# Optimization experiments

Measured on AMD Instinct MI355X. Metric: run time of the kernel, lower is better.

## Reference

```python
import jax, jax.numpy as jnp
import numpy as np

N_U, N_I, D = 30000, 15000, 64
L = 2                 # propagation layers (self.l)
TEMP = 0.2
LAMBDA1, LAMBDA2 = 0.2, 1e-7
H, F = 4, 16          # GAT heads x per-head dim; H*F == D
NEG_SLOPE = 0.2
AVG_DEG = 16
B = 2048


def setup_inputs() -> dict:
    key = jax.random.key(0)
    ks = jax.random.split(key, 10)
    rng = np.random.default_rng(0)
    E_u_0 = jax.random.normal(ks[0], (N_U, D), jnp.float32) * 0.1
    E_i_0 = jax.random.normal(ks[1], (N_I, D), jnp.float32) * 0.1
    # sparse normalized bipartite adjacency (adj_norm) as an edge list
    nnz = N_U * AVG_DEG
    u_idx = np.repeat(np.arange(N_U), AVG_DEG)
    i_idx = rng.integers(0, N_I, nnz)
    deg_u = np.bincount(u_idx, minlength=N_U)
    deg_i = np.maximum(np.bincount(i_idx, minlength=N_I), 1)
    vals = (1.0 / np.sqrt(deg_u[u_idx] * deg_i[i_idx])).astype(np.float32)
    # GAT graph on n_u+n_i nodes: bipartite edges both directions + self-loops
    n = N_U + N_I
    src = np.concatenate([u_idx, i_idx + N_U, np.arange(n)]).astype(np.int32)
    dst = np.concatenate([i_idx + N_U, u_idx, np.arange(n)]).astype(np.int32)
    # GAT parameters (fresh each forward in original, so just random)
    W = jax.random.normal(ks[2], (D, H * F), jnp.float32) / np.sqrt(D)
    attn_l = jax.random.normal(ks[3], (H, F), jnp.float32) * 0.1
    attn_r = jax.random.normal(ks[4], (H, F), jnp.float32) * 0.1
    uids = jax.random.randint(ks[5], (B,), 0, N_U, jnp.int32)
    iids = jax.random.randint(ks[6], (B,), 0, N_I, jnp.int32)
    pos = jax.random.randint(ks[7], (B,), 0, N_I, jnp.int32)
    neg = jax.random.randint(ks[8], (B,), 0, N_I, jnp.int32)
    return dict(E_u_0=E_u_0, E_i_0=E_i_0, adj_vals=jnp.asarray(vals),
                W=W, attn_l=attn_l, attn_r=attn_r,
                u_idx=jnp.asarray(u_idx, jnp.int32), i_idx=jnp.asarray(i_idx, jnp.int32),
                src=jnp.asarray(src), dst=jnp.asarray(dst),
                uids=uids, iids=iids, pos=pos, neg=neg)


def gat_layer(h, src, dst, W, attn_l, attn_r, n_nodes):
    # GATConv: project, per-edge attention, neighborhood softmax, scatter-agg
    feat = (h @ W).reshape(-1, H, F)                      # [N,H,F]
    el = (feat * attn_l).sum(-1)                          # [N,H]
    er = (feat * attn_r).sum(-1)                          # [N,H]
    e = jax.nn.leaky_relu(el[src] + er[dst], NEG_SLOPE)   # [E,H]
    e_max = jax.ops.segment_max(e, dst, num_segments=n_nodes)
    a = jnp.exp(e - e_max[dst])
    denom = jax.ops.segment_sum(a, dst, num_segments=n_nodes)
    a = a / denom[dst]                                    # self-loops => denom>0
    out = jax.ops.segment_sum(a[:, :, None] * feat[src], dst, num_segments=n_nodes)
    return jax.nn.elu(out.reshape(-1, H * F))             # [N,D]


def _forward(E_u_0, E_i_0, adj_vals, W, attn_l, attn_r,
             u_idx, i_idx, src, dst, uids, iids, pos, neg):
    n = N_U + N_I
    Eu, Ei = E_u_0, E_i_0
    sum_Eu, sum_Ei = E_u_0, E_i_0
    sum_Gu, sum_Gi = E_u_0, E_i_0
    for _ in range(L):
        # LightGCN spmm propagation: Z_u = A @ E_i, Z_i = A.T @ E_u
        Zu = jax.ops.segment_sum(adj_vals[:, None] * Ei[i_idx], u_idx, num_segments=N_U)
        Zi = jax.ops.segment_sum(adj_vals[:, None] * Eu[u_idx], i_idx, num_segments=N_I)
        ls1 = gat_layer(jnp.concatenate([Eu, Ei], 0), src, dst, W, attn_l, attn_r, n)
        Gu, Gi = ls1[:N_U], ls1[N_U:]
        Eu, Ei = Zu + Eu, Zi + Ei
        sum_Eu = sum_Eu + Eu
        sum_Ei = sum_Ei + Ei
        sum_Gu = sum_Gu + Gu
        sum_Gi = sum_Gi + Gi
    log_eps = jnp.float32(np.log(1e-8))
    # InfoNCE: log(sum(exp(s)) + 1e-8) == logaddexp(logsumexp(s), log(1e-8))
    lse_u = jax.scipy.special.logsumexp(sum_Gu[uids] @ sum_Eu.T / TEMP, axis=1)
    lse_i = jax.scipy.special.logsumexp(sum_Gi[iids] @ sum_Ei.T / TEMP, axis=1)
    neg_score = jnp.logaddexp(lse_u, log_eps).mean() + jnp.logaddexp(lse_i, log_eps).mean()
    pos_score = ((sum_Gu[uids] * sum_Eu[uids]).sum(1) / TEMP).mean() \
              + ((sum_Gi[iids] * sum_Ei[iids]).sum(1) / TEMP).mean()
    loss_s = -pos_score + neg_score
    # BPR loss
    u_emb = sum_Eu[uids]
    diff = (u_emb * sum_Ei[pos]).sum(-1) - (u_emb * sum_Ei[neg]).sum(-1)
    loss_r = -jax.nn.log_sigmoid(diff).mean()
    # L2 reg over nn.Parameters (E_u_0, E_i_0 only)
    loss_reg = LAMBDA2 * ((E_u_0 ** 2).sum() + (E_i_0 ** 2).sum())
    loss = loss_r + LAMBDA1 * loss_s + loss_reg
    return loss, loss_r, LAMBDA1 * loss_s


def reference(E_u_0, E_i_0, adj_vals, W, attn_l, attn_r,
              u_idx, i_idx, src, dst, uids, iids, pos, neg):
    return _forward(E_u_0, E_i_0, adj_vals, W, attn_l, attn_r,
                    u_idx, i_idx, src, dst, uids, iids, pos, neg)
```

## Files before the change

kernel.cpp:

```cpp
#include <hip/hip_runtime.h>
#include <math.h>

#define N_U 30000
#define N_I 15000
#define N_TOT 45000
#define D 64
#define NNZ 480000
#define B 2048
#define INV_TEMP 5.0f
#define LOG_EPS -18.420680743952367f
#define NEG_SLOPE 0.2f
#define LAMBDA1 0.2f
#define LAMBDA2 1e-7f

#define NSP 128
#define RSP_U 235
#define RSP_I 118
#define PAD_U 30016
#define PAD_I 15040
#define SCALE_LOG2 7.2134752044448170f
#define LN2F 0.6931471805599453f

typedef __attribute__((ext_vector_type(8))) short short8;
typedef __attribute__((ext_vector_type(4))) float f32x4;

__device__ inline float wred(float v) {
#pragma unroll
  for (int o = 32; o > 0; o >>= 1) v += __shfl_down(v, o, 64);
  return v;
}

__device__ inline float leaky(float v) { return (v >= 0.f) ? v : NEG_SLOPE * v; }

__device__ inline void atomMaxF(float* a, float v) {
  if (v >= 0.f) atomicMax((int*)a, __float_as_int(v));
  else atomicMin((unsigned int*)a, __float_as_uint(v));
}

__device__ inline unsigned short f2bf(float x) {
  unsigned u = __float_as_uint(x);
  unsigned r = u + 0x7FFFu + ((u >> 16) & 1u);
  return (unsigned short)(r >> 16);
}
__device__ inline float bf2f(unsigned short h) {
  return __uint_as_float(((unsigned)h) << 16);
}

__global__ void k_init(const float* __restrict__ Eu0, const float* __restrict__ Ei0,
                       float* fU, float* fI, float* sEu, float* sEi,
                       float* sGu, float* sGi, int* deg, float* acc) {
  int t = blockIdx.x * 256 + threadIdx.x;
  if (t < 16) acc[t] = (t >= 8) ? -INFINITY : 0.f;
  if (t < N_I) deg[t] = 0;
  if (t < N_U * D) {
    int n = t >> 6, c = t & 63;
    float v = Eu0[t];
    fU[(size_t)n * 128 + c] = v;
    sEu[t] = v; sGu[t] = v;
  } else if (t < N_TOT * D) {
    int j = t - N_U * D;
    int n = j >> 6, c = j & 63;
    float v = Ei0[j];
    fI[(size_t)n * 128 + c] = v;
    sEi[j] = v; sGi[j] = v;
  }
}

__global__ void k_deg(const int* __restrict__ ii, int* deg) {
  int e = blockIdx.x * 256 + threadIdx.x;
  if (e < NNZ) atomicAdd(&deg[ii[e]], 1);
}

__global__ void k_scan(const int* __restrict__ deg, int* rowptr, int* cursor) {
  __shared__ int buf[1024];
  __shared__ int carry;
  int tid = threadIdx.x;
  if (tid == 0) carry = 0;
  __syncthreads();
  for (int base = 0; base < N_I; base += 1024) {
    int v = (base + tid < N_I) ? deg[base + tid] : 0;
    buf[tid] = v;
    __syncthreads();
    for (int o = 1; o < 1024; o <<= 1) {
      int x = (tid >= o) ? buf[tid - o] : 0;
      __syncthreads();
      buf[tid] += x;
      __syncthreads();
    }
    if (base + tid < N_I) {
      int excl = carry + buf[tid] - v;
      rowptr[base + tid] = excl;
      cursor[base + tid] = excl;
    }
    __syncthreads();
    if (tid == 1023) carry += buf[1023];
    __syncthreads();
  }
  if (tid == 0) rowptr[N_I] = carry;
}

__global__ void k_fill(const int* __restrict__ ii, const float* __restrict__ vals,
                       int* cursor, int* u_srt, float* v_srt) {
  int e = blockIdx.x * 256 + threadIdx.x;
  if (e < NNZ) {
    int pos = atomicAdd(&cursor[ii[e]], 1);
    u_srt[pos] = e >> 4;
    v_srt[pos] = vals[e];
  }
}

__global__ void k_feat(float* __restrict__ fU, float* __restrict__ fI,
                       const float* __restrict__ W, const float* __restrict__ al,
                       const float* __restrict__ ar,
                       float* __restrict__ el, float* __restrict__ er) {
  __shared__ float Ws[64 * 64];
  __shared__ float hs[16][64];
  int tid = threadIdx.x;
  for (int t = tid; t < 1024; t += 256) ((float4*)Ws)[t] = ((const float4*)W)[t];
  int g = tid >> 6, c = tid & 63;
  int n0 = blockIdx.x * 16 + g * 4;
  float* rows[4];
#pragma unroll
  for (int j = 0; j < 4; j++) {
    int node = n0 + j;
    rows[j] = nullptr;
    if (node < N_TOT) {
      rows[j] = (node < N_U) ? (fU + (size_t)node * 128) : (fI + (size_t)(node - N_U) * 128);
      hs[g * 4 + j][c] = rows[j][c];
    }
  }
  __syncthreads();
  float a0 = 0.f, a1 = 0.f, a2 = 0.f, a3 = 0.f;
#pragma unroll 8
  for (int k = 0; k < 64; ++k) {
    float w = Ws[k * 64 + c];
    a0 = fmaf(hs[g * 4 + 0][k], w, a0);
    a1 = fmaf(hs[g * 4 + 1][k], w, a1);
    a2 = fmaf(hs[g * 4 + 2][k], w, a2);
    a3 = fmaf(hs[g * 4 + 3][k], w, a3);
  }
  float accs[4] = {a0, a1, a2, a3};
  float alc = al[c], arc = ar[c];
#pragma unroll
  for (int j = 0; j < 4; j++) {
    int node = n0 + j;
    if (node >= N_TOT) continue;
    rows[j][64 + c] = accs[j];
    float pl = accs[j] * alc;
    float pr = accs[j] * arc;
#pragma unroll
    for (int o = 8; o >= 1; o >>= 1) {
      pl += __shfl_down(pl, o, 16);
      pr += __shfl_down(pr, o, 16);
    }
    if ((c & 15) == 0) {
      el[node * 4 + (c >> 4)] = pl;
      er[node * 4 + (c >> 4)] = pr;
    }
  }
}

__global__ void k_elmax(const float* __restrict__ el, float* __restrict__ dst) {
  __shared__ float red[4][4];
  int tid = threadIdx.x;
  int lane = tid & 63, wv = tid >> 6;
  float mx = -INFINITY;
  for (int t = blockIdx.x * 256 + tid; t < N_TOT * 4; t += 64 * 256)
    mx = fmaxf(mx, el[t]);
#pragma unroll
  for (int o = 4; o < 64; o <<= 1) mx = fmaxf(mx, __shfl_xor(mx, o, 64));
  if (lane < 4) red[wv][lane] = mx;
  __syncthreads();
  if (tid < 4) {
    float m2 = fmaxf(fmaxf(red[0][tid], red[1][tid]), fmaxf(red[2][tid], red[3][tid]));
    atomMaxF(dst + tid, m2);
  }
}

__global__ void k_user_layer(const float* __restrict__ fU_cur, const float* __restrict__ fI_cur,
                             const float* __restrict__ el, const float* __restrict__ er,
                             const float* __restrict__ vals, const int* __restrict__ ii,
                             const float* __restrict__ elmx,
                             float* __restrict__ fU_nxt, float* __restrict__ sEu,
                             float* __restrict__ sGu,
                             unsigned short* __restrict__ EH, unsigned short* __restrict__ EL,
                             float* __restrict__ normArr) {
  int t = blockIdx.x * 256 + threadIdx.x;
  int u = t >> 6, c = t & 63;
  if (u >= N_U) return;
  int h = c >> 4;
  float eru = er[u * 4 + h];
  float m = leaky(elmx[h] + eru);
  const float* selfrow = fU_cur + (size_t)u * 128;
  float aself = __expf(leaky(el[u * 4 + h] + eru) - m);

  int idx[16]; float vv[16];
#pragma unroll
  for (int k = 0; k < 16; k++) { idx[k] = ii[u * 16 + k]; vv[k] = vals[u * 16 + k]; }
  float av[16];
#pragma unroll
  for (int k = 0; k < 16; k++)
    av[k] = __expf(leaky(el[(idx[k] + N_U) * 4 + h] + eru) - m);

  float den = aself;
#pragma unroll
  for (int k = 0; k < 16; k++) den += av[k];

  float o0 = aself * selfrow[64 + c], o1 = 0.f;
  float z0 = 0.f, z1 = 0.f;
#pragma unroll
  for (int k = 0; k < 16; k += 2) {
    const float* rA = fI_cur + (size_t)idx[k] * 128;
    const float* rB = fI_cur + (size_t)idx[k + 1] * 128;
    float eA = rA[c], fA = rA[64 + c];
    float eB = rB[c], fB = rB[64 + c];
    z0 = fmaf(vv[k], eA, z0);
    z1 = fmaf(vv[k + 1], eB, z1);
    o0 = fmaf(av[k], fA, o0);
    o1 = fmaf(av[k + 1], fB, o1);
  }
  float o = (o0 + o1) / den;
  float g = (o > 0.f) ? o : expm1f(o);
  float e_new = selfrow[c] + z0 + z1;
  fU_nxt[(size_t)u * 128 + c] = e_new;
  size_t off = (size_t)u * D + c;
  float s_final = sEu[off] + e_new;
  sEu[off] = s_final;
  sGu[off] += g;
  if (EH) {
    unsigned short hi = f2bf(s_final);
    EH[off] = hi;
    EL[off] = f2bf(s_final - bf2f(hi));
    float n2 = wred(s_final * s_final);
    if (c == 0) normArr[u] = n2;
  }
}

__global__ void k_item_layer(const float* __restrict__ fU_cur, const float* __restrict__ fI_cur,
                             const float* __restrict__ el, const float* __restrict__ er,
                             const int* __restrict__ rowptr, const int* __restrict__ u_srt,
                             const float* __restrict__ v_srt,
                             const float* __restrict__ elmx,
                             float* __restrict__ fI_nxt, float* __restrict__ sEi,
                             float* __restrict__ sGi,
                             unsigned short* __restrict__ EH, unsigned short* __restrict__ EL,
                             float* __restrict__ normArr) {
  int t = blockIdx.x * 256 + threadIdx.x;
  int i = t >> 6, c = t & 63;
  if (i >= N_I) return;
  int h = c >> 4;
  int node = N_U + i;
  float eri = er[node * 4 + h];
  float m = leaky(elmx[h] + eri);
  const float* selfrow = fI_cur + (size_t)i * 128;
  float aself = __expf(leaky(el[node * 4 + h] + eri) - m);
  float den0 = aself, den1 = 0.f;
  float o0 = aself * selfrow[64 + c], o1 = 0.f;
  float z0 = 0.f, z1 = 0.f;
  int r0 = rowptr[i], r1 = rowptr[i + 1];
  int r = r0;
  for (; r + 3 < r1; r += 4) {
    int u0 = u_srt[r], u1 = u_srt[r + 1], u2 = u_srt[r + 2], u3 = u_srt[r + 3];
    float v0 = v_srt[r], v1 = v_srt[r + 1], v2 = v_srt[r + 2], v3 = v_srt[r + 3];
    float a0 = __expf(leaky(el[u0 * 4 + h] + eri) - m);
    float a1 = __expf(leaky(el[u1 * 4 + h] + eri) - m);
    float a2 = __expf(leaky(el[u2 * 4 + h] + eri) - m);
    float a3 = __expf(leaky(el[u3 * 4 + h] + eri) - m);
    const float* R0 = fU_cur + (size_t)u0 * 128;
    const float* R1 = fU_cur + (size_t)u1 * 128;
    const float* R2 = fU_cur + (size_t)u2 * 128;
    const float* R3 = fU_cur + (size_t)u3 * 128;
    float e0 = R0[c], f0 = R0[64 + c];
    float e1 = R1[c], f1 = R1[64 + c];
    float e2 = R2[c], f2 = R2[64 + c];
    float e3 = R3[c], f3 = R3[64 + c];
    z0 = fmaf(v0, e0, z0); z1 = fmaf(v1, e1, z1);
    z0 = fmaf(v2, e2, z0); z1 = fmaf(v3, e3, z1);
    den0 += a0 + a2; den1 += a1 + a3;
    o0 = fmaf(a0, f0, o0); o1 = fmaf(a1, f1, o1);
    o0 = fmaf(a2, f2, o0); o1 = fmaf(a3, f3, o1);
  }
  for (; r < r1; r++) {
    int u0 = u_srt[r];
    float v0 = v_srt[r];
    float a0 = __expf(leaky(el[u0 * 4 + h] + eri) - m);
    const float* R0 = fU_cur + (size_t)u0 * 128;
    float e0 = R0[c], f0 = R0[64 + c];
    z0 = fmaf(v0, e0, z0);
    den0 += a0;
    o0 = fmaf(a0, f0, o0);
  }
  float o = (o0 + o1) / (den0 + den1);
  float g = (o > 0.f) ? o : expm1f(o);
  float e_new = selfrow[c] + z0 + z1;
  fI_nxt[(size_t)i * 128 + c] = e_new;
  size_t off = (size_t)i * D + c;
  float s_final = sEi[off] + e_new;
  sEi[off] = s_final;
  sGi[off] += g;
  if (EH) {
    unsigned short hi = f2bf(s_final);
    EH[off] = hi;
    EL[off] = f2bf(s_final - bf2f(hi));
    float n2 = wred(s_final * s_final);
    if (c == 0) normArr[i] = n2;
  }
}

__global__ void k_norm_max(const float* __restrict__ nU, const float* __restrict__ nI,
                           float* __restrict__ acc) {
  __shared__ float red[4][2];
  int tid = threadIdx.x;
  int lane = tid & 63, wv = tid >> 6;
  float mu = 0.f, mi = 0.f;
  for (int t = blockIdx.x * 256 + tid; t < N_U; t += 64 * 256) mu = fmaxf(mu, nU[t]);
  for (int t = blockIdx.x * 256 + tid; t < N_I; t += 64 * 256) mi = fmaxf(mi, nI[t]);
#pragma unroll
  for (int o = 32; o > 0; o >>= 1) {
    mu = fmaxf(mu, __shfl_down(mu, o, 64));
    mi = fmaxf(mi, __shfl_down(mi, o, 64));
  }
  if (lane == 0) { red[wv][0] = mu; red[wv][1] = mi; }
  __syncthreads();
  if (tid == 0) {
    float a = fmaxf(fmaxf(red[0][0], red[1][0]), fmaxf(red[2][0], red[3][0]));
    float b = fmaxf(fmaxf(red[0][1], red[1][1]), fmaxf(red[2][1], red[3][1]));
    atomMaxF(acc + 6, a);
    atomMaxF(acc + 7, b);
  }
}

__global__ void k_cvt_q(const float* __restrict__ sGu, const float* __restrict__ sGi,
                        const int* __restrict__ uids, const int* __restrict__ iids,
                        unsigned short* __restrict__ QuH, unsigned short* __restrict__ QuL,
                        unsigned short* __restrict__ QiH, unsigned short* __restrict__ QiL,
                        const float* __restrict__ acc,
                        float* __restrict__ M0u, float* __restrict__ M0i) {
  int lane = threadIdx.x & 63, wv = threadIdx.x >> 6;
  int row = blockIdx.x * 4 + wv;
  int side = row >> 11;
  int b = row & (B - 1);
  int id = side ? iids[b] : uids[b];
  float x = (side ? sGi : sGu)[(size_t)id * 64 + lane] * SCALE_LOG2;
  unsigned short hi = f2bf(x);
  unsigned short lo = f2bf(x - bf2f(hi));
  if (side) { QiH[(size_t)b * 64 + lane] = hi; QiL[(size_t)b * 64 + lane] = lo; }
  else      { QuH[(size_t)b * 64 + lane] = hi; QuL[(size_t)b * 64 + lane] = lo; }
  float n2 = wred(x * x);
  if (lane == 0) {
    float en2 = side ? acc[7] : acc[6];
    float M0 = sqrtf(n2) * sqrtf(en2) * 1.01f + 1.0f;
    (side ? M0i : M0u)[b] = M0;
  }
}

__global__ __launch_bounds__(256, 2) void k_lse_mfma(
    const unsigned short* __restrict__ Qhi, const unsigned short* __restrict__ Qlo,
    const unsigned short* __restrict__ Ehi, const unsigned short* __restrict__ Elo,
    const float* __restrict__ M0arr,
    int n_rows, int rows_per_split,
    float* __restrict__ part_s) {
  int tid = threadIdx.x;
  int wave = tid >> 6, lane = tid & 63;
  int l15 = lane & 15, quad = lane >> 4;
  int qbase = (blockIdx.x * 4 + wave) * 128;
  int split = blockIdx.y;
  int row0 = split * rows_per_split;
  int row_end = min(row0 + rows_per_split, n_rows);
  int rows = row_end - row0; if (rows < 0) rows = 0;
  int total = (rows + 15) >> 4;
  int ntail = rows & 15;

  float ss[8][4];
#pragma unroll
  for (int t = 0; t < 8; t++)
#pragma unroll
    for (int g = 0; g < 4; g++) ss[t][g] = 0.f;

  if (total > 0) {
    short8 ah[8][2], al[8][2];
#pragma unroll
    for (int t = 0; t < 8; t++)
#pragma unroll
      for (int c = 0; c < 2; c++) {
        size_t idx = (size_t)(qbase + t * 16 + l15) * 64 + c * 32 + quad * 8;
        ah[t][c] = *(const short8*)(Qhi + idx);
        al[t][c] = *(const short8*)(Qlo + idx);
      }

    f32x4 cinit[8];
#pragma unroll
    for (int t = 0; t < 8; t++)
#pragma unroll
      for (int g = 0; g < 4; g++)
        cinit[t][g] = -M0arr[qbase + t * 16 + quad * 4 + g];

    const unsigned short* ph = Ehi + (size_t)(row0 + l15) * 64 + quad * 8;
    const unsigned short* pl = Elo + (size_t)(row0 + l15) * 64 + quad * 8;

    short8 cb0 = *(const short8*)(ph);
    short8 cb1 = *(const short8*)(ph + 32);
    short8 cb2 = *(const short8*)(pl);
    short8 cb3 = *(const short8*)(pl + 32);
    ph += 1024; pl += 1024;

    for (int it = 0; it < total - 1; it++) {
      short8 nb0 = *(const short8*)(ph);
      short8 nb1 = *(const short8*)(ph + 32);
      short8 nb2 = *(const short8*)(pl);
      short8 nb3 = *(const short8*)(pl + 32);
      ph += 1024; pl += 1024;
#pragma unroll
      for (int t = 0; t < 8; t++) {
        f32x4 acc = cinit[t];
        acc = __builtin_amdgcn_mfma_f32_16x16x32_bf16(ah[t][0], cb0, acc, 0, 0, 0);
        acc = __builtin_amdgcn_mfma_f32_16x16x32_bf16(ah[t][1], cb1, acc, 0, 0, 0);
        acc = __builtin_amdgcn_mfma_f32_16x16x32_bf16(al[t][0], cb0, acc, 0, 0, 0);
        acc = __builtin_amdgcn_mfma_f32_16x16x32_bf16(al[t][1], cb1, acc, 0, 0, 0);
        acc = __builtin_amdgcn_mfma_f32_16x16x32_bf16(ah[t][0], cb2, acc, 0, 0, 0);
        acc = __builtin_amdgcn_mfma_f32_16x16x32_bf16(ah[t][1], cb3, acc, 0, 0, 0);
#pragma unroll
        for (int g = 0; g < 4; g++)
          ss[t][g] += exp2f(acc[g]);
      }
      cb0 = nb0; cb1 = nb1; cb2 = nb2; cb3 = nb3;
    }
    {
      bool valid = (ntail == 0) || (l15 < ntail);
#pragma unroll
      for (int t = 0; t < 8; t++) {
        f32x4 acc = cinit[t];
        acc = __builtin_amdgcn_mfma_f32_16x16x32_bf16(ah[t][0], cb0, acc, 0, 0, 0);
        acc = __builtin_amdgcn_mfma_f32_16x16x32_bf16(ah[t][1], cb1, acc, 0, 0, 0);
        acc = __builtin_amdgcn_mfma_f32_16x16x32_bf16(al[t][0], cb0, acc, 0, 0, 0);
        acc = __builtin_amdgcn_mfma_f32_16x16x32_bf16(al[t][1], cb1, acc, 0, 0, 0);
        acc = __builtin_amdgcn_mfma_f32_16x16x32_bf16(ah[t][0], cb2, acc, 0, 0, 0);
        acc = __builtin_amdgcn_mfma_f32_16x16x32_bf16(ah[t][1], cb3, acc, 0, 0, 0);
#pragma unroll
        for (int g = 0; g < 4; g++) {
          float e = exp2f(acc[g]);
          ss[t][g] += valid ? e : 0.f;
        }
      }
    }
  }

#pragma unroll
  for (int off = 1; off < 16; off <<= 1) {
#pragma unroll
    for (int t = 0; t < 8; t++)
#pragma unroll
      for (int g = 0; g < 4; g++)
        ss[t][g] += __shfl_xor(ss[t][g], off, 64);
  }

  if (l15 == 0) {
#pragma unroll
    for (int t = 0; t < 8; t++)
#pragma unroll
      for (int g = 0; g < 4; g++) {
        int q = qbase + t * 16 + quad * 4 + g;
        part_s[(size_t)split * B + q] = ss[t][g];
      }
  }
}

__global__ void k_reg(const float* __restrict__ Eu0, const float* __restrict__ Ei0, float* acc) {
  __shared__ float red[4];
  int tid = threadIdx.x;
  float s = 0.f;
  const float4* A = (const float4*)Eu0;
  const float4* Bp = (const float4*)Ei0;
  const int nA = N_U * 16, nTot = N_TOT * 16;
  for (int t = blockIdx.x * 256 + tid; t < nTot; t += 256 * 256) {
    float4 v = (t < nA) ? A[t] : Bp[t - nA];
    s += v.x * v.x + v.y * v.y + v.z * v.z + v.w * v.w;
  }
  s = wred(s);
  if ((tid & 63) == 0) red[tid >> 6] = s;
  __syncthreads();
  if (tid == 0) unsafeAtomicAdd(acc + 5, red[0] + red[1] + red[2] + red[3]);
}

__global__ void k_small(const float* __restrict__ sEu, const float* __restrict__ sEi,
                        const float* __restrict__ sGu, const float* __restrict__ sGi,
                        const int* __restrict__ uids, const int* __restrict__ iids,
                        const int* __restrict__ pos, const int* __restrict__ neg,
                        const float* __restrict__ psU, const float* __restrict__ psI,
                        const float* __restrict__ M0u, const float* __restrict__ M0i,
                        float* acc) {
  int b = blockIdx.x * 256 + threadIdx.x;
  float du = 0.f, di = 0.f, nu = 0.f, ni = 0.f, bpr = 0.f;
  if (b < B) {
    float su = 0.f, si = 0.f;
    for (int s2 = 0; s2 < NSP; s2++) su += psU[(size_t)s2 * B + b];
    for (int s2 = 0; s2 < NSP; s2++) si += psI[(size_t)s2 * B + b];
    float lseu = M0u[b] * LN2F + logf(su);
    float lsei = M0i[b] * LN2F + logf(si);
    nu = fmaxf(lseu, LOG_EPS) + log1pf(expf(-fabsf(lseu - LOG_EPS)));
    ni = fmaxf(lsei, LOG_EPS) + log1pf(expf(-fabsf(lsei - LOG_EPS)));

    int u = uids[b], it = iids[b], p = pos[b], ng = neg[b];
    const float4* gu = (const float4*)(sGu + (size_t)u * D);
    const float4* eu = (const float4*)(sEu + (size_t)u * D);
    const float4* gi = (const float4*)(sGi + (size_t)it * D);
    const float4* ei = (const float4*)(sEi + (size_t)it * D);
    const float4* ep = (const float4*)(sEi + (size_t)p * D);
    const float4* en = (const float4*)(sEi + (size_t)ng * D);
    float diff = 0.f;
#pragma unroll
    for (int k = 0; k < 16; k++) {
      float4 a = gu[k], b4 = eu[k];
      du += a.x * b4.x + a.y * b4.y + a.z * b4.z + a.w * b4.w;
      float4 c = gi[k], d4 = ei[k];
      di += c.x * d4.x + c.y * d4.y + c.z * d4.z + c.w * d4.w;
      float4 e = ep[k], f = en[k];
      diff += b4.x * (e.x - f.x) + b4.y * (e.y - f.y) + b4.z * (e.z - f.z) + b4.w * (e.w - f.w);
    }
    bpr = (diff > 0.f) ? log1pf(expf(-diff)) : (-diff + log1pf(expf(diff)));
  }
  du = wred(du); di = wred(di); nu = wred(nu); ni = wred(ni); bpr = wred(bpr);
  if ((threadIdx.x & 63) == 0) {
    unsafeAtomicAdd(acc + 0, du);
    unsafeAtomicAdd(acc + 1, di);
    unsafeAtomicAdd(acc + 2, nu);
    unsafeAtomicAdd(acc + 3, ni);
    unsafeAtomicAdd(acc + 4, bpr);
  }
}

__global__ void k_final(const float* __restrict__ acc, float* __restrict__ out) {
  float pos_score = (acc[0] + acc[1]) * (INV_TEMP / (float)B);
  float neg_score = (acc[2] + acc[3]) / (float)B;
  float loss_s = neg_score - pos_score;
  float loss_r = acc[4] / (float)B;
  float reg = LAMBDA2 * acc[5];
  out[0] = loss_r + LAMBDA1 * loss_s + reg;
  out[1] = loss_r;
  out[2] = LAMBDA1 * loss_s;
}

extern "C" void kernel_launch(void* const* d_in, const int* in_sizes, int n_in,
                              void* d_out, int out_size, void* d_ws, size_t ws_size,
                              hipStream_t stream) {
  const float* Eu0  = (const float*)d_in[0];
  const float* Ei0  = (const float*)d_in[1];
  const float* vals = (const float*)d_in[2];
  const float* W    = (const float*)d_in[3];
  const float* al   = (const float*)d_in[4];
  const float* ar   = (const float*)d_in[5];
  const int* ii     = (const int*)d_in[7];
  const int* uids   = (const int*)d_in[10];
  const int* iids   = (const int*)d_in[11];
  const int* pos    = (const int*)d_in[12];
  const int* neg    = (const int*)d_in[13];
  float* out = (float*)d_out;

  char* base = (char*)d_ws;
  size_t off = 0;
  auto alloc = [&](size_t bytes) -> void* {
    void* p = base + off;
    off = (off + bytes + 255) & ~(size_t)255;
    return p;
  };
  float* fU_a = (float*)alloc((size_t)N_U * 128 * 4);
  float* fU_b = (float*)alloc((size_t)N_U * 128 * 4);
  float* fI_a = (float*)alloc((size_t)N_I * 128 * 4);
  float* fI_b = (float*)alloc((size_t)N_I * 128 * 4);
  float* sEu  = (float*)alloc((size_t)N_U * D * 4);
  float* sEi  = (float*)alloc((size_t)N_I * D * 4);
  float* sGu  = (float*)alloc((size_t)N_U * D * 4);
  float* sGi  = (float*)alloc((size_t)N_I * D * 4);
  float* el   = (float*)alloc((size_t)N_TOT * 4 * 4);
  float* er   = (float*)alloc((size_t)N_TOT * 4 * 4);
  float* psU  = (float*)alloc((size_t)B * NSP * 4);
  float* psI  = (float*)alloc((size_t)B * NSP * 4);
  float* M0u  = (float*)alloc((size_t)B * 4);
  float* M0i  = (float*)alloc((size_t)B * 4);
  float* normU= (float*)alloc((size_t)N_U * 4);
  float* normI= (float*)alloc((size_t)N_I * 4);
  float* acc  = (float*)alloc(16 * 4);
  int* deg    = (int*)alloc((size_t)N_I * 4);
  int* cursor = (int*)alloc((size_t)N_I * 4);
  int* rowptr = (int*)alloc((size_t)(N_I + 1) * 4);
  int* u_srt  = (int*)alloc((size_t)NNZ * 4);
  float* v_srt= (float*)alloc((size_t)NNZ * 4);
  unsigned short* EuH = (unsigned short*)alloc((size_t)PAD_U * 64 * 2);
  unsigned short* EuL = (unsigned short*)alloc((size_t)PAD_U * 64 * 2);
  unsigned short* EiH = (unsigned short*)alloc((size_t)PAD_I * 64 * 2);
  unsigned short* EiL = (unsigned short*)alloc((size_t)PAD_I * 64 * 2);
  unsigned short* QuH = (unsigned short*)alloc((size_t)B * 64 * 2);
  unsigned short* QuL = (unsigned short*)alloc((size_t)B * 64 * 2);
  unsigned short* QiH = (unsigned short*)alloc((size_t)B * 64 * 2);
  unsigned short* QiL = (unsigned short*)alloc((size_t)B * 64 * 2);

  k_init<<<(N_TOT * D + 255) / 256, 256, 0, stream>>>(Eu0, Ei0, fU_a, fI_a, sEu, sEi, sGu, sGi,
                                                      deg, acc);
  k_deg<<<(NNZ + 255) / 256, 256, 0, stream>>>(ii, deg);
  k_scan<<<1, 1024, 0, stream>>>(deg, rowptr, cursor);
  k_fill<<<(NNZ + 255) / 256, 256, 0, stream>>>(ii, vals, cursor, u_srt, v_srt);

  float* cu = fU_a; float* ci = fI_a;
  float* nu = fU_b; float* ni = fI_b;
  for (int l = 0; l < 2; ++l) {
    float* elmx = acc + 8 + 4 * l;
    bool last = (l == 1);
    k_feat<<<(N_TOT + 15) / 16, 256, 0, stream>>>(cu, ci, W, al, ar, el, er);
    k_elmax<<<64, 256, 0, stream>>>(el, elmx);
    k_user_layer<<<(N_U * D) / 256, 256, 0, stream>>>(cu, ci, el, er, vals, ii, elmx, nu, sEu, sGu,
                                                      last ? EuH : nullptr, last ? EuL : nullptr,
                                                      normU);
    k_item_layer<<<(N_I * D) / 256, 256, 0, stream>>>(cu, ci, el, er, rowptr, u_srt, v_srt, elmx,
                                                      ni, sEi, sGi,
                                                      last ? EiH : nullptr, last ? EiL : nullptr,
                                                      normI);
    float* t1 = cu; cu = nu; nu = t1;
    float* t2 = ci; ci = ni; ni = t2;
  }

  k_norm_max<<<64, 256, 0, stream>>>(normU, normI, acc);
  k_cvt_q<<<(2 * B) / 4, 256, 0, stream>>>(sGu, sGi, uids, iids, QuH, QuL, QiH, QiL, acc, M0u, M0i);
  k_lse_mfma<<<dim3(B / 512, NSP), 256, 0, stream>>>(QuH, QuL, EuH, EuL, M0u, N_U, RSP_U, psU);
  k_lse_mfma<<<dim3(B / 512, NSP), 256, 0, stream>>>(QiH, QiL, EiH, EiL, M0i, N_I, RSP_I, psI);
  k_reg<<<256, 256, 0, stream>>>(Eu0, Ei0, acc);
  k_small<<<B / 256, 256, 0, stream>>>(sEu, sEi, sGu, sGi, uids, iids, pos, neg,
                                       psU, psI, M0u, M0i, acc);
  k_final<<<1, 1, 0, stream>>>(acc, out);
}
```

Measured before the change: 464.3 us.

## Merge per-layer user/item kernels, fuse reg into norm-max, batch LSE launches

Combines the user and item propagation kernels into one launch covering all nodes. Folds the L2 regularization sum into the norm-max reduction kernel, and launches both LSE MFMA passes as a single grid using blockIdx.z. Also rewrites the degree scan so each thread sums a chunk of 15 elements, replacing the serial 15-pass block scan. The aim is to cut launch count and tail idle time between small kernels. The cost is branch divergence at the user/item boundary and more registers held in the merged kernel.

```diff
diff --git a/kernel.cpp b/kernel.cpp
--- a/kernel.cpp
+++ b/kernel.cpp
@@ -72,31 +72,35 @@
 }
 
 __global__ void k_scan(const int* __restrict__ deg, int* rowptr, int* cursor) {
-  __shared__ int buf[1024];
-  __shared__ int carry;
+  __shared__ int tsum[1024];
+  const int CHUNK = 15;
   int tid = threadIdx.x;
-  if (tid == 0) carry = 0;
+  int base = tid * CHUNK;
+  int s = 0;
+#pragma unroll
+  for (int k = 0; k < CHUNK; k++) {
+    int idx = base + k;
+    s += (idx < N_I) ? deg[idx] : 0;
+  }
+  tsum[tid] = s;
   __syncthreads();
-  for (int base = 0; base < N_I; base += 1024) {
-    int v = (base + tid < N_I) ? deg[base + tid] : 0;
-    buf[tid] = v;
+  for (int o = 1; o < 1024; o <<= 1) {
+    int x = (tid >= o) ? tsum[tid - o] : 0;
     __syncthreads();
-    for (int o = 1; o < 1024; o <<= 1) {
-      int x = (tid >= o) ? buf[tid - o] : 0;
-      __syncthreads();
-      buf[tid] += x;
-      __syncthreads();
-    }
-    if (base + tid < N_I) {
-      int excl = carry + buf[tid] - v;
-      rowptr[base + tid] = excl;
-      cursor[base + tid] = excl;
-    }
+    tsum[tid] += x;
     __syncthreads();
-    if (tid == 1023) carry += buf[1023];
-    __syncthreads();
-  }
-  if (tid == 0) rowptr[N_I] = carry;
+  }
+  int excl = tsum[tid] - s;
+#pragma unroll
+  for (int k = 0; k < CHUNK; k++) {
+    int idx = base + k;
+    if (idx < N_I) {
+      rowptr[idx] = excl;
+      cursor[idx] = excl;
+      excl += deg[idx];
+    }
+  }
+  if (tid == 1023) rowptr[N_I] = tsum[1023];
 }
 
 __global__ void k_fill(const int* __restrict__ ii, const float* __restrict__ vals,
@@ -177,156 +181,161 @@
   }
 }
 
-__global__ void k_user_layer(const float* __restrict__ fU_cur, const float* __restrict__ fI_cur,
-                             const float* __restrict__ el, const float* __restrict__ er,
-                             const float* __restrict__ vals, const int* __restrict__ ii,
-                             const float* __restrict__ elmx,
-                             float* __restrict__ fU_nxt, float* __restrict__ sEu,
-                             float* __restrict__ sGu,
-                             unsigned short* __restrict__ EH, unsigned short* __restrict__ EL,
-                             float* __restrict__ normArr) {
+__global__ void k_layer(const float* __restrict__ fU_cur, const float* __restrict__ fI_cur,
+                        const float* __restrict__ el, const float* __restrict__ er,
+                        const float* __restrict__ vals, const int* __restrict__ ii,
+                        const int* __restrict__ rowptr, const int* __restrict__ u_srt,
+                        const float* __restrict__ v_srt,
+                        const float* __restrict__ elmx,
+                        float* __restrict__ fU_nxt, float* __restrict__ fI_nxt,
+                        float* __restrict__ sEu, float* __restrict__ sEi,
+                        float* __restrict__ sGu, float* __restrict__ sGi,
+                        unsigned short* __restrict__ EuH, unsigned short* __restrict__ EuL,
+                        unsigned short* __restrict__ EiH, unsigned short* __restrict__ EiL,
+                        float* __restrict__ normU, float* __restrict__ normI) {
   int t = blockIdx.x * 256 + threadIdx.x;
-  int u = t >> 6, c = t & 63;
-  if (u >= N_U) return;
+  int node = t >> 6, c = t & 63;
+  if (node >= N_TOT) return;
   int h = c >> 4;
-  float eru = er[u * 4 + h];
-  float m = leaky(elmx[h] + eru);
-  const float* selfrow = fU_cur + (size_t)u * 128;
-  float aself = __expf(leaky(el[u * 4 + h] + eru) - m);
-
-  int idx[16]; float vv[16];
-#pragma unroll
-  for (int k = 0; k < 16; k++) { idx[k] = ii[u * 16 + k]; vv[k] = vals[u * 16 + k]; }
-  float av[16];
-#pragma unroll
-  for (int k = 0; k < 16; k++)
-    av[k] = __expf(leaky(el[(idx[k] + N_U) * 4 + h] + eru) - m);
-
-  float den = aself;
-#pragma unroll
-  for (int k = 0; k < 16; k++) den += av[k];
-
-  float o0 = aself * selfrow[64 + c], o1 = 0.f;
-  float z0 = 0.f, z1 = 0.f;
-#pragma unroll
-  for (int k = 0; k < 16; k += 2) {
-    const float* rA = fI_cur + (size_t)idx[k] * 128;
-    const float* rB = fI_cur + (size_t)idx[k + 1] * 128;
-    float eA = rA[c], fA = rA[64 + c];
-    float eB = rB[c], fB = rB[64 + c];
-    z0 = fmaf(vv[k], eA, z0);
-    z1 = fmaf(vv[k + 1], eB, z1);
-    o0 = fmaf(av[k], fA, o0);
-    o1 = fmaf(av[k + 1], fB, o1);
-  }
-  float o = (o0 + o1) / den;
-  float g = (o > 0.f) ? o : expm1f(o);
-  float e_new = selfrow[c] + z0 + z1;
-  fU_nxt[(size_t)u * 128 + c] = e_new;
-  size_t off = (size_t)u * D + c;
-  float s_final = sEu[off] + e_new;
-  sEu[off] = s_final;
-  sGu[off] += g;
-  if (EH) {
-    unsigned short hi = f2bf(s_final);
-    EH[off] = hi;
-    EL[off] = f2bf(s_final - bf2f(hi));
-    float n2 = wred(s_final * s_final);
-    if (c == 0) normArr[u] = n2;
-  }
-}
-
-__global__ void k_item_layer(const float* __restrict__ fU_cur, const float* __restrict__ fI_cur,
-                             const float* __restrict__ el, const float* __restrict__ er,
-                             const int* __restrict__ rowptr, const int* __restrict__ u_srt,
-                             const float* __restrict__ v_srt,
-                             const float* __restrict__ elmx,
-                             float* __restrict__ fI_nxt, float* __restrict__ sEi,
-                             float* __restrict__ sGi,
-                             unsigned short* __restrict__ EH, unsigned short* __restrict__ EL,
-                             float* __restrict__ normArr) {
-  int t = blockIdx.x * 256 + threadIdx.x;
-  int i = t >> 6, c = t & 63;
-  if (i >= N_I) return;
-  int h = c >> 4;
-  int node = N_U + i;
-  float eri = er[node * 4 + h];
-  float m = leaky(elmx[h] + eri);
-  const float* selfrow = fI_cur + (size_t)i * 128;
-  float aself = __expf(leaky(el[node * 4 + h] + eri) - m);
-  float den0 = aself, den1 = 0.f;
-  float o0 = aself * selfrow[64 + c], o1 = 0.f;
-  float z0 = 0.f, z1 = 0.f;
-  int r0 = rowptr[i], r1 = rowptr[i + 1];
-  int r = r0;
-  for (; r + 3 < r1; r += 4) {
-    int u0 = u_srt[r], u1 = u_srt[r + 1], u2 = u_srt[r + 2], u3 = u_srt[r + 3];
-    float v0 = v_srt[r], v1 = v_srt[r + 1], v2 = v_srt[r + 2], v3 = v_srt[r + 3];
-    float a0 = __expf(leaky(el[u0 * 4 + h] + eri) - m);
-    float a1 = __expf(leaky(el[u1 * 4 + h] + eri) - m);
-    float a2 = __expf(leaky(el[u2 * 4 + h] + eri) - m);
-    float a3 = __expf(leaky(el[u3 * 4 + h] + eri) - m);
-    const float* R0 = fU_cur + (size_t)u0 * 128;
-    const float* R1 = fU_cur + (size_t)u1 * 128;
-    const float* R2 = fU_cur + (size_t)u2 * 128;
-    const float* R3 = fU_cur + (size_t)u3 * 128;
-    float e0 = R0[c], f0 = R0[64 + c];
-    float e1 = R1[c], f1 = R1[64 + c];
-    float e2 = R2[c], f2 = R2[64 + c];
-    float e3 = R3[c], f3 = R3[64 + c];
-    z0 = fmaf(v0, e0, z0); z1 = fmaf(v1, e1, z1);
-    z0 = fmaf(v2, e2, z0); z1 = fmaf(v3, e3, z1);
-    den0 += a0 + a2; den1 += a1 + a3;
-    o0 = fmaf(a0, f0, o0); o1 = fmaf(a1, f1, o1);
-    o0 = fmaf(a2, f2, o0); o1 = fmaf(a3, f3, o1);
-  }
-  for (; r < r1; r++) {
-    int u0 = u_srt[r];
-    float v0 = v_srt[r];
-    float a0 = __expf(leaky(el[u0 * 4 + h] + eri) - m);
-    const float* R0 = fU_cur + (size_t)u0 * 128;
-    float e0 = R0[c], f0 = R0[64 + c];
-    z0 = fmaf(v0, e0, z0);
-    den0 += a0;
-    o0 = fmaf(a0, f0, o0);
-  }
-  float o = (o0 + o1) / (den0 + den1);
-  float g = (o > 0.f) ? o : expm1f(o);
-  float e_new = selfrow[c] + z0 + z1;
-  fI_nxt[(size_t)i * 128 + c] = e_new;
-  size_t off = (size_t)i * D + c;
-  float s_final = sEi[off] + e_new;
-  sEi[off] = s_final;
-  sGi[off] += g;
-  if (EH) {
-    unsigned short hi = f2bf(s_final);
-    EH[off] = hi;
-    EL[off] = f2bf(s_final - bf2f(hi));
-    float n2 = wred(s_final * s_final);
-    if (c == 0) normArr[i] = n2;
-  }
-}
-
-__global__ void k_norm_max(const float* __restrict__ nU, const float* __restrict__ nI,
-                           float* __restrict__ acc) {
-  __shared__ float red[4][2];
+
+  if (node < N_U) {
+    int u = node;
+    float eru = er[u * 4 + h];
+    float m = leaky(elmx[h] + eru);
+    const float* selfrow = fU_cur + (size_t)u * 128;
+    float aself = __expf(leaky(el[u * 4 + h] + eru) - m);
+
+    int idx[16]; float vv[16];
+#pragma unroll
+    for (int k = 0; k < 16; k++) { idx[k] = ii[u * 16 + k]; vv[k] = vals[u * 16 + k]; }
+    float av[16];
+#pragma unroll
+    for (int k = 0; k < 16; k++)
+      av[k] = __expf(leaky(el[(idx[k] + N_U) * 4 + h] + eru) - m);
+
+    float den = aself;
+#pragma unroll
+    for (int k = 0; k < 16; k++) den += av[k];
+
+    float o0 = aself * selfrow[64 + c], o1 = 0.f;
+    float z0 = 0.f, z1 = 0.f;
+#pragma unroll
+    for (int k = 0; k < 16; k += 2) {
+      const float* rA = fI_cur + (size_t)idx[k] * 128;
+      const float* rB = fI_cur + (size_t)idx[k + 1] * 128;
+      float eA = rA[c], fA = rA[64 + c];
+      float eB = rB[c], fB = rB[64 + c];
+      z0 = fmaf(vv[k], eA, z0);
+      z1 = fmaf(vv[k + 1], eB, z1);
+      o0 = fmaf(av[k], fA, o0);
+      o1 = fmaf(av[k + 1], fB, o1);
+    }
+    float o = (o0 + o1) / den;
+    float g = (o > 0.f) ? o : expm1f(o);
+    float e_new = selfrow[c] + z0 + z1;
+    fU_nxt[(size_t)u * 128 + c] = e_new;
+    size_t off = (size_t)u * D + c;
+    float s_final = sEu[off] + e_new;
+    sEu[off] = s_final;
+    sGu[off] += g;
+    if (EuH) {
+      unsigned short hi = f2bf(s_final);
+      EuH[off] = hi;
+      EuL[off] = f2bf(s_final - bf2f(hi));
+      float n2 = wred(s_final * s_final);
+      if (c == 0) normU[u] = n2;
+    }
+  } else {
+    int i = node - N_U;
+    float eri = er[node * 4 + h];
+    float m = leaky(elmx[h] + eri);
+    const float* selfrow = fI_cur + (size_t)i * 128;
+    float aself = __expf(leaky(el[node * 4 + h] + eri) - m);
+    float den0 = aself, den1 = 0.f;
+    float o0 = aself * selfrow[64 + c], o1 = 0.f;
+    float z0 = 0.f, z1 = 0.f;
+    int r0 = rowptr[i], r1 = rowptr[i + 1];
+    int r = r0;
+    for (; r + 3 < r1; r += 4) {
+      int u0 = u_srt[r], u1 = u_srt[r + 1], u2 = u_srt[r + 2], u3 = u_srt[r + 3];
+      float v0 = v_srt[r], v1 = v_srt[r + 1], v2 = v_srt[r + 2], v3 = v_srt[r + 3];
+      float a0 = __expf(leaky(el[u0 * 4 + h] + eri) - m);
+      float a1 = __expf(leaky(el[u1 * 4 + h] + eri) - m);
+      float a2 = __expf(leaky(el[u2 * 4 + h] + eri) - m);
+      float a3 = __expf(leaky(el[u3 * 4 + h] + eri) - m);
+      const float* R0 = fU_cur + (size_t)u0 * 128;
+      const float* R1 = fU_cur + (size_t)u1 * 128;
+      const float* R2 = fU_cur + (size_t)u2 * 128;
+      const float* R3 = fU_cur + (size_t)u3 * 128;
+      float e0 = R0[c], f0 = R0[64 + c];
+      float e1 = R1[c], f1 = R1[64 + c];
+      float e2 = R2[c], f2 = R2[64 + c];
+      float e3 = R3[c], f3 = R3[64 + c];
+      z0 = fmaf(v0, e0, z0); z1 = fmaf(v1, e1, z1);
+      z0 = fmaf(v2, e2, z0); z1 = fmaf(v3, e3, z1);
+      den0 += a0 + a2; den1 += a1 + a3;
+      o0 = fmaf(a0, f0, o0); o1 = fmaf(a1, f1, o1);
+      o0 = fmaf(a2, f2, o0); o1 = fmaf(a3, f3, o1);
+    }
+    for (; r < r1; r++) {
+      int u0 = u_srt[r];
+      float v0 = v_srt[r];
+      float a0 = __expf(leaky(el[u0 * 4 + h] + eri) - m);
+      const float* R0 = fU_cur + (size_t)u0 * 128;
+      float e0 = R0[c], f0 = R0[64 + c];
+      z0 = fmaf(v0, e0, z0);
+      den0 += a0;
+      o0 = fmaf(a0, f0, o0);
+    }
+    float o = (o0 + o1) / (den0 + den1);
+    float g = (o > 0.f) ? o : expm1f(o);
+    float e_new = selfrow[c] + z0 + z1;
+    fI_nxt[(size_t)i * 128 + c] = e_new;
+    size_t off = (size_t)i * D + c;
+    float s_final = sEi[off] + e_new;
+    sEi[off] = s_final;
+    sGi[off] += g;
+    if (EiH) {
+      unsigned short hi = f2bf(s_final);
+      EiH[off] = hi;
+      EiL[off] = f2bf(s_final - bf2f(hi));
+      float n2 = wred(s_final * s_final);
+      if (c == 0) normI[i] = n2;
+    }
+  }
+}
+
+__global__ void k_normreg(const float* __restrict__ nU, const float* __restrict__ nI,
+                          const float* __restrict__ Eu0, const float* __restrict__ Ei0,
+                          float* __restrict__ acc) {
+  __shared__ float red[4][3];
   int tid = threadIdx.x;
   int lane = tid & 63, wv = tid >> 6;
-  float mu = 0.f, mi = 0.f;
-  for (int t = blockIdx.x * 256 + tid; t < N_U; t += 64 * 256) mu = fmaxf(mu, nU[t]);
-  for (int t = blockIdx.x * 256 + tid; t < N_I; t += 64 * 256) mi = fmaxf(mi, nI[t]);
+  float mu = 0.f, mi = 0.f, s = 0.f;
+  for (int t = blockIdx.x * 256 + tid; t < N_U; t += 128 * 256) mu = fmaxf(mu, nU[t]);
+  for (int t = blockIdx.x * 256 + tid; t < N_I; t += 128 * 256) mi = fmaxf(mi, nI[t]);
+  const float4* A = (const float4*)Eu0;
+  const float4* Bp = (const float4*)Ei0;
+  const int nA = N_U * 16, nTot = N_TOT * 16;
+  for (int t = blockIdx.x * 256 + tid; t < nTot; t += 128 * 256) {
+    float4 v = (t < nA) ? A[t] : Bp[t - nA];
+    s += v.x * v.x + v.y * v.y + v.z * v.z + v.w * v.w;
+  }
 #pragma unroll
   for (int o = 32; o > 0; o >>= 1) {
     mu = fmaxf(mu, __shfl_down(mu, o, 64));
     mi = fmaxf(mi, __shfl_down(mi, o, 64));
-  }
-  if (lane == 0) { red[wv][0] = mu; red[wv][1] = mi; }
+    s += __shfl_down(s, o, 64);
+  }
+  if (lane == 0) { red[wv][0] = mu; red[wv][1] = mi; red[wv][2] = s; }
   __syncthreads();
   if (tid == 0) {
     float a = fmaxf(fmaxf(red[0][0], red[1][0]), fmaxf(red[2][0], red[3][0]));
     float b = fmaxf(fmaxf(red[0][1], red[1][1]), fmaxf(red[2][1], red[3][1]));
+    float ssum = red[0][2] + red[1][2] + red[2][2] + red[3][2];
     atomMaxF(acc + 6, a);
     atomMaxF(acc + 7, b);
+    unsafeAtomicAdd(acc + 5, ssum);
   }
 }
 
@@ -355,11 +364,22 @@
 }
 
 __global__ __launch_bounds__(256, 2) void k_lse_mfma(
-    const unsigned short* __restrict__ Qhi, const unsigned short* __restrict__ Qlo,
-    const unsigned short* __restrict__ Ehi, const unsigned short* __restrict__ Elo,
-    const float* __restrict__ M0arr,
-    int n_rows, int rows_per_split,
-    float* __restrict__ part_s) {
+    const unsigned short* __restrict__ QuH, const unsigned short* __restrict__ QuL,
+    const unsigned short* __restrict__ EuHp, const unsigned short* __restrict__ EuLp,
+    const unsigned short* __restrict__ QiH, const unsigned short* __restrict__ QiL,
+    const unsigned short* __restrict__ EiHp, const unsigned short* __restrict__ EiLp,
+    const float* __restrict__ M0u, const float* __restrict__ M0i,
+    float* __restrict__ psU, float* __restrict__ psI) {
+  int z = blockIdx.z;
+  const unsigned short* Qhi = z ? QiH : QuH;
+  const unsigned short* Qlo = z ? QiL : QuL;
+  const unsigned short* Ehi = z ? EiHp : EuHp;
+  const unsigned short* Elo = z ? EiLp : EuLp;
+  const float* M0arr = z ? M0i : M0u;
+  float* part_s = z ? psI : psU;
+  int n_rows = z ? N_I : N_U;
+  int rows_per_split = z ? RSP_I : RSP_U;
+
   int tid = threadIdx.x;
   int wave = tid >> 6, lane = tid & 63;
   int l15 = lane & 15, quad = lane >> 4;
@@ -463,23 +483,6 @@
         part_s[(size_t)split * B + q] = ss[t][g];
       }
   }
-}
-
-__global__ void k_reg(const float* __restrict__ Eu0, const float* __restrict__ Ei0, float* acc) {
-  __shared__ float red[4];
-  int tid = threadIdx.x;
-  float s = 0.f;
-  const float4* A = (const float4*)Eu0;
-  const float4* Bp = (const float4*)Ei0;
-  const int nA = N_U * 16, nTot = N_TOT * 16;
-  for (int t = blockIdx.x * 256 + tid; t < nTot; t += 256 * 256) {
-    float4 v = (t < nA) ? A[t] : Bp[t - nA];
-    s += v.x * v.x + v.y * v.y + v.z * v.z + v.w * v.w;
-  }
-  s = wred(s);
-  if ((tid & 63) == 0) red[tid >> 6] = s;
-  __syncthreads();
-  if (tid == 0) unsafeAtomicAdd(acc + 5, red[0] + red[1] + red[2] + red[3]);
 }
 
 __global__ void k_small(const float* __restrict__ sEu, const float* __restrict__ sEi,
@@ -607,22 +610,21 @@
     bool last = (l == 1);
     k_feat<<<(N_TOT + 15) / 16, 256, 0, stream>>>(cu, ci, W, al, ar, el, er);
     k_elmax<<<64, 256, 0, stream>>>(el, elmx);
-    k_user_layer<<<(N_U * D) / 256, 256, 0, stream>>>(cu, ci, el, er, vals, ii, elmx, nu, sEu, sGu,
-                                                      last ? EuH : nullptr, last ? EuL : nullptr,
-                                                      normU);
-    k_item_layer<<<(N_I * D) / 256, 256, 0, stream>>>(cu, ci, el, er, rowptr, u_srt, v_srt, elmx,
-                                                      ni, sEi, sGi,
-                                                      last ? EiH : nullptr, last ? EiL : nullptr,
-                                                      normI);
+    k_layer<<<(N_TOT * D) / 256, 256, 0, stream>>>(
+        cu, ci, el, er, vals, ii, rowptr, u_srt, v_srt, elmx,
+        nu, ni, sEu, sEi, sGu, sGi,
+        last ? EuH : nullptr, last ? EuL : nullptr,
+        last ? EiH : nullptr, last ? EiL : nullptr,
+        normU, normI);
     float* t1 = cu; cu = nu; nu = t1;
     float* t2 = ci; ci = ni; ni = t2;
   }
 
-  k_norm_max<<<64, 256, 0, stream>>>(normU, normI, acc);
+  k_normreg<<<128, 256, 0, stream>>>(normU, normI, Eu0, Ei0, acc);
   k_cvt_q<<<(2 * B) / 4, 256, 0, stream>>>(sGu, sGi, uids, iids, QuH, QuL, QiH, QiL, acc, M0u, M0i);
-  k_lse_mfma<<<dim3(B / 512, NSP), 256, 0, stream>>>(QuH, QuL, EuH, EuL, M0u, N_U, RSP_U, psU);
-  k_lse_mfma<<<dim3(B / 512, NSP), 256, 0, stream>>>(QiH, QiL, EiH, EiL, M0i, N_I, RSP_I, psI);
-  k_reg<<<256, 256, 0, stream>>>(Eu0, Ei0, acc);
+  k_lse_mfma<<<dim3(B / 512, NSP, 2), 256, 0, stream>>>(QuH, QuL, EuH, EuL,
+                                                        QiH, QiL, EiH, EiL,
+                                                        M0u, M0i, psU, psI);
   k_small<<<B / 256, 256, 0, stream>>>(sEu, sEi, sGu, sGi, uids, iids, pos, neg,
                                        psU, psI, M0u, M0i, acc);
   k_final<<<1, 1, 0, stream>>>(acc, out);
```

After: 446.0 us. -4.0%, faster.
